# Optimization experiments

Measured on AMD Instinct MI355X. Metric: run time of the kernel, lower is better.

## Reference

```python
import jax, jax.numpy as jnp
import numpy as np
import math

B, T, D_IN, D_OUT = 4, 2048, 2048, 2048

def _inv_sigmoid(v):
    return math.log(v / (1 - v + 1e-08))

def setup_inputs() -> dict:
    key = jax.random.key(0)
    ks = jax.random.split(key, 6)
    x = jax.random.normal(ks[0], (B, T, D_IN), dtype=jnp.float32)
    W_p = jax.random.normal(ks[1], (D_OUT, D_IN), dtype=jnp.float32) * 0.02
    W_i = jax.random.normal(ks[2], (D_OUT, D_IN), dtype=jnp.float32) * 0.002
    W_d = jax.random.normal(ks[3], (D_OUT, D_IN), dtype=jnp.float32) * 0.002
    alpha_logit = jnp.full((D_IN,), _inv_sigmoid(0.9), dtype=jnp.float32)
    beta_logit = jnp.full((D_IN,), _inv_sigmoid(0.5), dtype=jnp.float32)
    W_gate_w = jax.random.normal(ks[4], (3, 3 * D_IN), dtype=jnp.float32) * 0.01
    W_gate_b = jnp.array([1.0, 0.0, 0.0], dtype=jnp.float32)
    bias = jnp.zeros((D_OUT,), dtype=jnp.float32)
    return {"x": x, "W_p": W_p, "W_i": W_i, "W_d": W_d,
            "alpha_logit": alpha_logit, "beta_logit": beta_logit,
            "W_gate_w": W_gate_w, "W_gate_b": W_gate_b, "bias": bias}

def _pid_features(x, alpha, beta):
    # x: (B,T,D). Single scan computing EMA integral and smoothed derivative.
    x_t = jnp.swapaxes(x, 0, 1)  # (T,B,D)
    x_prev = jnp.concatenate([jnp.zeros_like(x_t[:1]), x_t[:-1]], axis=0)
    diff_t = x_t - x_prev  # raw finite difference
    def step(carry, inp):
        s, d = carry
        xt, dt = inp
        s = alpha * s + (1.0 - alpha) * xt
        d = beta * d + (1.0 - beta) * dt
        return (s, d), (s, d)
    s0 = jnp.zeros(x.shape[::2], dtype=x.dtype)  # (B,D)
    _, (integ_t, deriv_t) = jax.lax.scan(step, (s0, s0), (x_t, diff_t))
    return jnp.swapaxes(integ_t, 0, 1), jnp.swapaxes(deriv_t, 0, 1)

def reference(x, W_p, W_i, W_d, alpha_logit, beta_logit, W_gate_w, W_gate_b, bias):
    alpha = jax.nn.sigmoid(alpha_logit)  # (D,)
    beta = jax.nn.sigmoid(beta_logit)
    integral, derivative = _pid_features(x, alpha, beta)  # (B,T,D) each
    gate_in = jnp.concatenate([x, integral, derivative], axis=-1)  # (B,T,3D)
    logits = jnp.einsum('btk,gk->btg', gate_in, W_gate_w) + W_gate_b
    gates = jax.nn.softmax(logits, axis=-1)  # (B,T,3)
    p_out = jnp.einsum('btd,od->bto', x, W_p)
    i_out = jnp.einsum('btd,od->bto', integral, W_i)
    d_out = jnp.einsum('btd,od->bto', derivative, W_d)
    y = gates[..., 0:1] * p_out + gates[..., 1:2] * i_out + gates[..., 2:3] * d_out + bias
    return y
```

## Files before the change

### kernel.cpp

```cpp
#include <hip/hip_runtime.h>
#include <stdint.h>

typedef unsigned short u16;

#define GAS __attribute__((address_space(1)))
#define LAS __attribute__((address_space(3)))

typedef __bf16 bf16x8 __attribute__((ext_vector_type(8)));
typedef float f32x4 __attribute__((ext_vector_type(4)));


__device__ inline u16 f2b(float f) {
    uint32_t x = __float_as_uint(f);
    uint32_t r = (x + 0x7fffu + ((x >> 16) & 1u)) >> 16;
    return (u16)r;
}

__device__ inline float b2f(u16 u) {
    union { uint32_t i; float f; } v;
    v.i = ((uint32_t)u) << 16;
    return v.f;
}

__device__ inline void load8b(float* v, const u16* p) {
    uint4 u = *(const uint4*)p;
    v[0] = b2f((u16)(u.x)); v[1] = b2f((u16)(u.x >> 16));
    v[2] = b2f((u16)(u.y)); v[3] = b2f((u16)(u.y >> 16));
    v[4] = b2f((u16)(u.z)); v[5] = b2f((u16)(u.z >> 16));
    v[6] = b2f((u16)(u.w)); v[7] = b2f((u16)(u.w >> 16));
}

__device__ inline void load8f(float* v, const float* p) {
    float4 a = *(const float4*)p;
    float4 b = *(const float4*)(p + 4);
    v[0] = a.x; v[1] = a.y; v[2] = a.z; v[3] = a.w;
    v[4] = b.x; v[5] = b.y; v[6] = b.z; v[7] = b.w;
}

__device__ inline void store8b(u16* p, const float* v, float scale) {
    uint4 u;
    u.x = (uint32_t)f2b(v[0] * scale) | ((uint32_t)f2b(v[1] * scale) << 16);
    u.y = (uint32_t)f2b(v[2] * scale) | ((uint32_t)f2b(v[3] * scale) << 16);
    u.z = (uint32_t)f2b(v[4] * scale) | ((uint32_t)f2b(v[5] * scale) << 16);
    u.w = (uint32_t)f2b(v[6] * scale) | ((uint32_t)f2b(v[7] * scale) << 16);
    *(uint4*)p = u;
}

__device__ inline float sigmoidf(float v) { return 1.f / (1.f + __expf(-v)); }

__device__ inline float pow64f(float a) {
    float p = a * a;
    p = p * p;
    p = p * p;
    p = p * p;
    p = p * p;
    return p * p;
}

__device__ inline float* carry_ptr(u16* Z, int plane, int b, int c, int d) {
    int f = ((plane * 4 + b) * 32 + c) * 2048 + d;
    int row = f >> 10;
    int off = f & 1023;
    return (float*)(Z + (size_t)row * 6144) + off;
}

__global__ __launch_bounds__(256) void pack_w(
    const float* __restrict__ Wp, const float* __restrict__ Wi,
    const float* __restrict__ Wd, u16* __restrict__ Wcat)
{
    int i = (blockIdx.x * 256 + threadIdx.x) * 8;
    int seg = i >> 22;
    int j = i & 4194303;
    const float* src = (seg == 0) ? Wp : (seg == 1) ? Wi : Wd;
    int o = j >> 11;
    int c = j & 2047;
    float v[8];
    load8f(v, src + j);
    store8b(Wcat + (size_t)o * 6144 + seg * 2048 + c, v, 1.0f);
}

__global__ __launch_bounds__(256) void scan_pass1(
    const float* __restrict__ x, const float* __restrict__ alog,
    const float* __restrict__ blog, u16* __restrict__ Z)
{
    const int d = blockIdx.x * 256 + threadIdx.x;
    const int c = blockIdx.y;
    const int b = blockIdx.z;
    const float alpha = sigmoidf(alog[d]);
    const float beta  = sigmoidf(blog[d]);
    const float oma = 1.f - alpha, omb = 1.f - beta;
    const float* xp = x + ((size_t)b * 2048 + c * 64) * 2048 + d;
    float xprev = (c == 0) ? 0.f : xp[-2048];
    float s = 0.f, dd = 0.f;
    #pragma unroll 8
    for (int t = 0; t < 64; ++t) {
        float xf = xp[(size_t)t * 2048];
        s = alpha * s + oma * xf;
        dd = beta * dd + omb * (xf - xprev);
        xprev = xf;
    }
    *carry_ptr(Z, 0, b, c, d) = s;
    *carry_ptr(Z, 1, b, c, d) = dd;
}

__global__ __launch_bounds__(256) void scan_pass2(
    const float* __restrict__ alog, const float* __restrict__ blog,
    u16* __restrict__ Z)
{
    const int g = blockIdx.x * 256 + threadIdx.x;
    const int b = g >> 11;
    const int d = g & 2047;
    const float aL = pow64f(sigmoidf(alog[d]));
    const float bL = pow64f(sigmoidf(blog[d]));
    float sIn = 0.f, dIn = 0.f;
    for (int c = 0; c < 32; ++c) {
        float* sp = carry_ptr(Z, 0, b, c, d);
        float* dp = carry_ptr(Z, 1, b, c, d);
        float sl = *sp, dl = *dp;
        *sp = sIn; *dp = dIn;
        sIn = sl + aL * sIn;
        dIn = dl + bL * dIn;
    }
}

__global__ __launch_bounds__(256) void scan_pass3(
    const float* __restrict__ x, const float* __restrict__ alog,
    const float* __restrict__ blog, u16* __restrict__ Z)
{
    const int d = blockIdx.x * 256 + threadIdx.x;
    const int c = blockIdx.y;
    const int b = blockIdx.z;
    const float alpha = sigmoidf(alog[d]);
    const float beta  = sigmoidf(blog[d]);
    const float oma = 1.f - alpha, omb = 1.f - beta;
    const float* xp = x + ((size_t)b * 2048 + c * 64) * 2048 + d;
    u16* zp = Z + ((size_t)b * 2048 + c * 64) * 6144 + 2048 + d;
    float s  = *carry_ptr(Z, 0, b, c, d);
    float dd = *carry_ptr(Z, 1, b, c, d);
    float xprev = (c == 0) ? 0.f : xp[-2048];
    #pragma unroll 8
    for (int t = 0; t < 64; ++t) {
        float xf = xp[(size_t)t * 2048];
        s = alpha * s + oma * xf;
        dd = beta * dd + omb * (xf - xprev);
        xprev = xf;
        size_t zo = (size_t)t * 6144;
        zp[zo] = f2b(s);
        zp[zo + 2048] = f2b(dd);
    }
}

__global__ __launch_bounds__(256) void gates_kernel(
    const float* __restrict__ x, const float* __restrict__ Wg,
    const float* __restrict__ Wgb, u16* __restrict__ Z)
{
    const int row = blockIdx.x;
    const int tid = threadIdx.x;
    const int k = tid * 8;
    const float* xr = x + (size_t)row * 2048;
    u16* zr = Z + (size_t)row * 6144;

    float xv[8], sv[8], dv[8];
    load8f(xv, xr + k);
    load8b(sv, zr + 2048 + k);
    load8b(dv, zr + 4096 + k);

    float p[3];
    #pragma unroll
    for (int gg = 0; gg < 3; ++gg) {
        float wx[8], ws[8], wd[8];
        load8f(wx, Wg + gg * 6144 + k);
        load8f(ws, Wg + gg * 6144 + 2048 + k);
        load8f(wd, Wg + gg * 6144 + 4096 + k);
        float acc = 0.f;
        #pragma unroll
        for (int j = 0; j < 8; ++j)
            acc += xv[j] * wx[j] + sv[j] * ws[j] + dv[j] * wd[j];
        p[gg] = acc;
    }

    #pragma unroll
    for (int off = 32; off > 0; off >>= 1) {
        p[0] += __shfl_down(p[0], off);
        p[1] += __shfl_down(p[1], off);
        p[2] += __shfl_down(p[2], off);
    }

    __shared__ float red[4][3];
    __shared__ float gsh[3];
    int wv = tid >> 6, lane = tid & 63;
    if (lane == 0) { red[wv][0] = p[0]; red[wv][1] = p[1]; red[wv][2] = p[2]; }
    __syncthreads();
    if (tid == 0) {
        float l0 = red[0][0] + red[1][0] + red[2][0] + red[3][0] + Wgb[0];
        float l1 = red[0][1] + red[1][1] + red[2][1] + red[3][1] + Wgb[1];
        float l2 = red[0][2] + red[1][2] + red[2][2] + red[3][2] + Wgb[2];
        float m = fmaxf(l0, fmaxf(l1, l2));
        float e0 = __expf(l0 - m), e1 = __expf(l1 - m), e2 = __expf(l2 - m);
        float inv = 1.f / (e0 + e1 + e2);
        gsh[0] = e0 * inv; gsh[1] = e1 * inv; gsh[2] = e2 * inv;
    }
    __syncthreads();
    float g0 = gsh[0], g1 = gsh[1], g2 = gsh[2];
    store8b(zr + k, xv, g0);
    store8b(zr + 2048 + k, sv, g1);
    store8b(zr + 4096 + k, dv, g2);
}

__global__ __launch_bounds__(256, 3) void gemm_kernel(
    const u16* __restrict__ Z, const u16* __restrict__ Wcat,
    const float* __restrict__ bias, float* __restrict__ out)
{
    __shared__ u16 a_sh[128 * 64];
    __shared__ u16 b_sh[128 * 64];

    const int tid = threadIdx.x;
    const int bm = blockIdx.y * 128;
    const int bn = blockIdx.x * 128;

    const int srow = tid >> 3;
    const int scq  = tid & 7;
    const int ssub = (scq ^ (srow & 7)) * 8;
    const u16* aglob = Z + (size_t)(bm + srow) * 6144 + ssub;
    const u16* bglob = Wcat + (size_t)(bn + srow) * 6144 + ssub;
    u16* alds[4];
    u16* blds[4];
    #pragma unroll
    for (int c = 0; c < 4; ++c) {
        alds[c] = a_sh + c * 2048 + tid * 8;
        blds[c] = b_sh + c * 2048 + tid * 8;
    }

    const int lane = tid & 63;
    const int wv = tid >> 6;
    const int wm = (wv & 1) * 64;
    const int wn = (wv >> 1) * 64;
    const int fr = lane & 15;
    const int fq = lane >> 4;

    f32x4 acc[4][4] = {};

    for (int kt = 0; kt < 96; ++kt) {
        const int k0 = kt * 64;
        #pragma unroll
        for (int c = 0; c < 4; ++c)
            __builtin_amdgcn_global_load_lds(
                (const GAS uint32_t*)(aglob + (size_t)c * 32 * 6144 + k0),
                (LAS uint32_t*)alds[c], 16, 0, 0);
        #pragma unroll
        for (int c = 0; c < 4; ++c)
            __builtin_amdgcn_global_load_lds(
                (const GAS uint32_t*)(bglob + (size_t)c * 32 * 6144 + k0),
                (LAS uint32_t*)blds[c], 16, 0, 0);
        __syncthreads();

        #pragma unroll
        for (int h = 0; h < 2; ++h) {
            bf16x8 avf[4], bvf[4];
            #pragma unroll
            for (int i = 0; i < 4; ++i) {
                int row = wm + i * 16 + fr;
                int ch = (fq + 4 * h) ^ (row & 7);
                avf[i] = *(const bf16x8*)(a_sh + row * 64 + ch * 8);
            }
            #pragma unroll
            for (int j = 0; j < 4; ++j) {
                int row = wn + j * 16 + fr;
                int ch = (fq + 4 * h) ^ (row & 7);
                bvf[j] = *(const bf16x8*)(b_sh + row * 64 + ch * 8);
            }
            #pragma unroll
            for (int i = 0; i < 4; ++i)
                #pragma unroll
                for (int j = 0; j < 4; ++j)
                    acc[i][j] = __builtin_amdgcn_mfma_f32_16x16x32_bf16(
                        avf[i], bvf[j], acc[i][j], 0, 0, 0);
        }
        __syncthreads();
    }

    #pragma unroll
    for (int j = 0; j < 4; ++j) {
        const int col = bn + wn + j * 16 + fr;
        const float bv = bias[col];
        #pragma unroll
        for (int i = 0; i < 4; ++i) {
            const int row0 = bm + wm + i * 16 + fq * 4;
            #pragma unroll
            for (int r = 0; r < 4; ++r)
                out[(size_t)(row0 + r) * 2048 + col] = acc[i][j][r] + bv;
        }
    }
}

extern "C" void kernel_launch(void* const* d_in, const int* in_sizes, int n_in,
                              void* d_out, int out_size, void* d_ws, size_t ws_size,
                              hipStream_t stream) {
    const float* x    = (const float*)d_in[0];
    const float* Wp   = (const float*)d_in[1];
    const float* Wi   = (const float*)d_in[2];
    const float* Wd   = (const float*)d_in[3];
    const float* al   = (const float*)d_in[4];
    const float* bl   = (const float*)d_in[5];
    const float* Wg   = (const float*)d_in[6];
    const float* Wgb  = (const float*)d_in[7];
    const float* bias = (const float*)d_in[8];
    float* out = (float*)d_out;

    u16* Z    = (u16*)d_ws;
    u16* Wcat = (u16*)((char*)d_ws + (size_t)8192 * 6144 * 2);

    pack_w<<<6144, 256, 0, stream>>>(Wp, Wi, Wd, Wcat);
    scan_pass1<<<dim3(8, 32, 4), 256, 0, stream>>>(x, al, bl, Z);
    scan_pass2<<<32, 256, 0, stream>>>(al, bl, Z);
    scan_pass3<<<dim3(8, 32, 4), 256, 0, stream>>>(x, al, bl, Z);
    gates_kernel<<<8192, 256, 0, stream>>>(x, Wg, Wgb, Z);
    gemm_kernel<<<dim3(16, 64), 256, 0, stream>>>(Z, Wcat, bias, out);
}
```

Measured before the change: 442.7 us.

## Fuse gate logits into scan pass and apply gates as GEMM epilogue scaling

Removes the separate gates kernel. The scan now writes x, integral and derivative as unscaled bf16 into Z and accumulates the gate logits through wave reductions and atomics. A small softmax kernel turns the logits into gates. The GEMM applies the per-row gates by rescaling the accumulators between K segments with ratios g0/g1 and g1/g2, then multiplying by g2 in the epilogue. This avoids one full read and rewrite of Z, at the cost of per-timestep wave shuffles and atomics in the scan, plus division-based rescaling that can lose precision or blow up when a gate is tiny.

```diff
diff --git a/kernel.cpp b/kernel.cpp
--- a/kernel.cpp
+++ b/kernel.cpp
@@ -14,20 +14,6 @@
     uint32_t x = __float_as_uint(f);
     uint32_t r = (x + 0x7fffu + ((x >> 16) & 1u)) >> 16;
     return (u16)r;
-}
-
-__device__ inline float b2f(u16 u) {
-    union { uint32_t i; float f; } v;
-    v.i = ((uint32_t)u) << 16;
-    return v.f;
-}
-
-__device__ inline void load8b(float* v, const u16* p) {
-    uint4 u = *(const uint4*)p;
-    v[0] = b2f((u16)(u.x)); v[1] = b2f((u16)(u.x >> 16));
-    v[2] = b2f((u16)(u.y)); v[3] = b2f((u16)(u.y >> 16));
-    v[4] = b2f((u16)(u.z)); v[5] = b2f((u16)(u.z >> 16));
-    v[6] = b2f((u16)(u.w)); v[7] = b2f((u16)(u.w >> 16));
 }
 
 __device__ inline void load8f(float* v, const float* p) {
@@ -37,12 +23,12 @@
     v[4] = b.x; v[5] = b.y; v[6] = b.z; v[7] = b.w;
 }
 
-__device__ inline void store8b(u16* p, const float* v, float scale) {
+__device__ inline void store8b(u16* p, const float* v) {
     uint4 u;
-    u.x = (uint32_t)f2b(v[0] * scale) | ((uint32_t)f2b(v[1] * scale) << 16);
-    u.y = (uint32_t)f2b(v[2] * scale) | ((uint32_t)f2b(v[3] * scale) << 16);
-    u.z = (uint32_t)f2b(v[4] * scale) | ((uint32_t)f2b(v[5] * scale) << 16);
-    u.w = (uint32_t)f2b(v[6] * scale) | ((uint32_t)f2b(v[7] * scale) << 16);
+    u.x = (uint32_t)f2b(v[0]) | ((uint32_t)f2b(v[1]) << 16);
+    u.y = (uint32_t)f2b(v[2]) | ((uint32_t)f2b(v[3]) << 16);
+    u.z = (uint32_t)f2b(v[4]) | ((uint32_t)f2b(v[5]) << 16);
+    u.w = (uint32_t)f2b(v[6]) | ((uint32_t)f2b(v[7]) << 16);
     *(uint4*)p = u;
 }
 
@@ -55,13 +41,6 @@
     p = p * p;
     p = p * p;
     return p * p;
-}
-
-__device__ inline float* carry_ptr(u16* Z, int plane, int b, int c, int d) {
-    int f = ((plane * 4 + b) * 32 + c) * 2048 + d;
-    int row = f >> 10;
-    int off = f & 1023;
-    return (float*)(Z + (size_t)row * 6144) + off;
 }
 
 __global__ __launch_bounds__(256) void pack_w(
@@ -76,12 +55,12 @@
     int c = j & 2047;
     float v[8];
     load8f(v, src + j);
-    store8b(Wcat + (size_t)o * 6144 + seg * 2048 + c, v, 1.0f);
+    store8b(Wcat + (size_t)o * 6144 + seg * 2048 + c, v);
 }
 
 __global__ __launch_bounds__(256) void scan_pass1(
     const float* __restrict__ x, const float* __restrict__ alog,
-    const float* __restrict__ blog, u16* __restrict__ Z)
+    const float* __restrict__ blog, float* __restrict__ carries)
 {
     const int d = blockIdx.x * 256 + threadIdx.x;
     const int c = blockIdx.y;
@@ -99,13 +78,13 @@
         dd = beta * dd + omb * (xf - xprev);
         xprev = xf;
     }
-    *carry_ptr(Z, 0, b, c, d) = s;
-    *carry_ptr(Z, 1, b, c, d) = dd;
+    carries[((0 * 4 + b) * 32 + c) * 2048 + d] = s;
+    carries[((1 * 4 + b) * 32 + c) * 2048 + d] = dd;
 }
 
 __global__ __launch_bounds__(256) void scan_pass2(
     const float* __restrict__ alog, const float* __restrict__ blog,
-    u16* __restrict__ Z)
+    float* __restrict__ carries)
 {
     const int g = blockIdx.x * 256 + threadIdx.x;
     const int b = g >> 11;
@@ -114,8 +93,8 @@
     const float bL = pow64f(sigmoidf(blog[d]));
     float sIn = 0.f, dIn = 0.f;
     for (int c = 0; c < 32; ++c) {
-        float* sp = carry_ptr(Z, 0, b, c, d);
-        float* dp = carry_ptr(Z, 1, b, c, d);
+        float* sp = carries + ((0 * 4 + b) * 32 + c) * 2048 + d;
+        float* dp = carries + ((1 * 4 + b) * 32 + c) * 2048 + d;
         float sl = *sp, dl = *dp;
         *sp = sIn; *dp = dIn;
         sIn = sl + aL * sIn;
@@ -125,7 +104,9 @@
 
 __global__ __launch_bounds__(256) void scan_pass3(
     const float* __restrict__ x, const float* __restrict__ alog,
-    const float* __restrict__ blog, u16* __restrict__ Z)
+    const float* __restrict__ blog, const float* __restrict__ Wg,
+    const float* __restrict__ carries, u16* __restrict__ Z,
+    float* __restrict__ logits)
 {
     const int d = blockIdx.x * 256 + threadIdx.x;
     const int c = blockIdx.y;
@@ -133,83 +114,63 @@
     const float alpha = sigmoidf(alog[d]);
     const float beta  = sigmoidf(blog[d]);
     const float oma = 1.f - alpha, omb = 1.f - beta;
+    const float w0x = Wg[d],         w0s = Wg[2048 + d],         w0d = Wg[4096 + d];
+    const float w1x = Wg[6144 + d],  w1s = Wg[6144 + 2048 + d],  w1d = Wg[6144 + 4096 + d];
+    const float w2x = Wg[12288 + d], w2s = Wg[12288 + 2048 + d], w2d = Wg[12288 + 4096 + d];
     const float* xp = x + ((size_t)b * 2048 + c * 64) * 2048 + d;
-    u16* zp = Z + ((size_t)b * 2048 + c * 64) * 6144 + 2048 + d;
-    float s  = *carry_ptr(Z, 0, b, c, d);
-    float dd = *carry_ptr(Z, 1, b, c, d);
+    u16* zp = Z + ((size_t)b * 2048 + c * 64) * 6144 + d;
+    float s  = carries[((0 * 4 + b) * 32 + c) * 2048 + d];
+    float dd = carries[((1 * 4 + b) * 32 + c) * 2048 + d];
     float xprev = (c == 0) ? 0.f : xp[-2048];
-    #pragma unroll 8
+    const int rowbase = b * 2048 + c * 64;
+    const int lane = threadIdx.x & 63;
+    #pragma unroll 4
     for (int t = 0; t < 64; ++t) {
         float xf = xp[(size_t)t * 2048];
         s = alpha * s + oma * xf;
         dd = beta * dd + omb * (xf - xprev);
         xprev = xf;
         size_t zo = (size_t)t * 6144;
-        zp[zo] = f2b(s);
-        zp[zo + 2048] = f2b(dd);
-    }
-}
-
-__global__ __launch_bounds__(256) void gates_kernel(
-    const float* __restrict__ x, const float* __restrict__ Wg,
-    const float* __restrict__ Wgb, u16* __restrict__ Z)
-{
-    const int row = blockIdx.x;
-    const int tid = threadIdx.x;
-    const int k = tid * 8;
-    const float* xr = x + (size_t)row * 2048;
-    u16* zr = Z + (size_t)row * 6144;
-
-    float xv[8], sv[8], dv[8];
-    load8f(xv, xr + k);
-    load8b(sv, zr + 2048 + k);
-    load8b(dv, zr + 4096 + k);
-
-    float p[3];
-    #pragma unroll
-    for (int gg = 0; gg < 3; ++gg) {
-        float wx[8], ws[8], wd[8];
-        load8f(wx, Wg + gg * 6144 + k);
-        load8f(ws, Wg + gg * 6144 + 2048 + k);
-        load8f(wd, Wg + gg * 6144 + 4096 + k);
-        float acc = 0.f;
+        zp[zo]        = f2b(xf);
+        zp[zo + 2048] = f2b(s);
+        zp[zo + 4096] = f2b(dd);
+        float c0 = w0x * xf + w0s * s + w0d * dd;
+        float c1 = w1x * xf + w1s * s + w1d * dd;
+        float c2 = w2x * xf + w2s * s + w2d * dd;
         #pragma unroll
-        for (int j = 0; j < 8; ++j)
-            acc += xv[j] * wx[j] + sv[j] * ws[j] + dv[j] * wd[j];
-        p[gg] = acc;
-    }
-
-    #pragma unroll
-    for (int off = 32; off > 0; off >>= 1) {
-        p[0] += __shfl_down(p[0], off);
-        p[1] += __shfl_down(p[1], off);
-        p[2] += __shfl_down(p[2], off);
-    }
-
-    __shared__ float red[4][3];
-    __shared__ float gsh[3];
-    int wv = tid >> 6, lane = tid & 63;
-    if (lane == 0) { red[wv][0] = p[0]; red[wv][1] = p[1]; red[wv][2] = p[2]; }
-    __syncthreads();
-    if (tid == 0) {
-        float l0 = red[0][0] + red[1][0] + red[2][0] + red[3][0] + Wgb[0];
-        float l1 = red[0][1] + red[1][1] + red[2][1] + red[3][1] + Wgb[1];
-        float l2 = red[0][2] + red[1][2] + red[2][2] + red[3][2] + Wgb[2];
-        float m = fmaxf(l0, fmaxf(l1, l2));
-        float e0 = __expf(l0 - m), e1 = __expf(l1 - m), e2 = __expf(l2 - m);
-        float inv = 1.f / (e0 + e1 + e2);
-        gsh[0] = e0 * inv; gsh[1] = e1 * inv; gsh[2] = e2 * inv;
-    }
-    __syncthreads();
-    float g0 = gsh[0], g1 = gsh[1], g2 = gsh[2];
-    store8b(zr + k, xv, g0);
-    store8b(zr + 2048 + k, sv, g1);
-    store8b(zr + 4096 + k, dv, g2);
+        for (int off = 32; off > 0; off >>= 1) {
+            c0 += __shfl_xor(c0, off);
+            c1 += __shfl_xor(c1, off);
+            c2 += __shfl_xor(c2, off);
+        }
+        if (lane == 0) {
+            int row = rowbase + t;
+            atomicAdd(&logits[row * 3 + 0], c0);
+            atomicAdd(&logits[row * 3 + 1], c1);
+            atomicAdd(&logits[row * 3 + 2], c2);
+        }
+    }
+}
+
+__global__ __launch_bounds__(256) void softmax_k(
+    float* __restrict__ logits, const float* __restrict__ Wgb)
+{
+    int r = blockIdx.x * 256 + threadIdx.x;
+    float l0 = logits[r * 3 + 0] + Wgb[0];
+    float l1 = logits[r * 3 + 1] + Wgb[1];
+    float l2 = logits[r * 3 + 2] + Wgb[2];
+    float m = fmaxf(l0, fmaxf(l1, l2));
+    float e0 = __expf(l0 - m), e1 = __expf(l1 - m), e2 = __expf(l2 - m);
+    float inv = 1.f / (e0 + e1 + e2);
+    logits[r * 3 + 0] = e0 * inv;
+    logits[r * 3 + 1] = e1 * inv;
+    logits[r * 3 + 2] = e2 * inv;
 }
 
 __global__ __launch_bounds__(256, 3) void gemm_kernel(
     const u16* __restrict__ Z, const u16* __restrict__ Wcat,
-    const float* __restrict__ bias, float* __restrict__ out)
+    const float* __restrict__ gates, const float* __restrict__ bias,
+    float* __restrict__ out)
 {
     __shared__ u16 a_sh[128 * 64];
     __shared__ u16 b_sh[128 * 64];
@@ -238,45 +199,74 @@
     const int fr = lane & 15;
     const int fq = lane >> 4;
 
+    float r01[16], r12[16], g2v[16];
+    #pragma unroll
+    for (int i = 0; i < 4; ++i) {
+        #pragma unroll
+        for (int r = 0; r < 4; ++r) {
+            int row = bm + wm + i * 16 + fq * 4 + r;
+            float g0 = gates[row * 3 + 0];
+            float g1 = gates[row * 3 + 1];
+            float g2 = gates[row * 3 + 2];
+            int idx = i * 4 + r;
+            r01[idx] = g0 / g1;
+            r12[idx] = g1 / g2;
+            g2v[idx] = g2;
+        }
+    }
+
     f32x4 acc[4][4] = {};
 
-    for (int kt = 0; kt < 96; ++kt) {
-        const int k0 = kt * 64;
-        #pragma unroll
-        for (int c = 0; c < 4; ++c)
-            __builtin_amdgcn_global_load_lds(
-                (const GAS uint32_t*)(aglob + (size_t)c * 32 * 6144 + k0),
-                (LAS uint32_t*)alds[c], 16, 0, 0);
-        #pragma unroll
-        for (int c = 0; c < 4; ++c)
-            __builtin_amdgcn_global_load_lds(
-                (const GAS uint32_t*)(bglob + (size_t)c * 32 * 6144 + k0),
-                (LAS uint32_t*)blds[c], 16, 0, 0);
-        __syncthreads();
-
-        #pragma unroll
-        for (int h = 0; h < 2; ++h) {
-            bf16x8 avf[4], bvf[4];
-            #pragma unroll
-            for (int i = 0; i < 4; ++i) {
-                int row = wm + i * 16 + fr;
-                int ch = (fq + 4 * h) ^ (row & 7);
-                avf[i] = *(const bf16x8*)(a_sh + row * 64 + ch * 8);
+    for (int seg = 0; seg < 3; ++seg) {
+        for (int kt = 0; kt < 32; ++kt) {
+            const int k0 = seg * 2048 + kt * 64;
+            #pragma unroll
+            for (int c = 0; c < 4; ++c)
+                __builtin_amdgcn_global_load_lds(
+                    (const GAS uint32_t*)(aglob + (size_t)c * 32 * 6144 + k0),
+                    (LAS uint32_t*)alds[c], 16, 0, 0);
+            #pragma unroll
+            for (int c = 0; c < 4; ++c)
+                __builtin_amdgcn_global_load_lds(
+                    (const GAS uint32_t*)(bglob + (size_t)c * 32 * 6144 + k0),
+                    (LAS uint32_t*)blds[c], 16, 0, 0);
+            __syncthreads();
+
+            #pragma unroll
+            for (int h = 0; h < 2; ++h) {
+                bf16x8 avf[4], bvf[4];
+                #pragma unroll
+                for (int i = 0; i < 4; ++i) {
+                    int row = wm + i * 16 + fr;
+                    int ch = (fq + 4 * h) ^ (row & 7);
+                    avf[i] = *(const bf16x8*)(a_sh + row * 64 + ch * 8);
+                }
+                #pragma unroll
+                for (int j = 0; j < 4; ++j) {
+                    int row = wn + j * 16 + fr;
+                    int ch = (fq + 4 * h) ^ (row & 7);
+                    bvf[j] = *(const bf16x8*)(b_sh + row * 64 + ch * 8);
+                }
+                #pragma unroll
+                for (int i = 0; i < 4; ++i)
+                    #pragma unroll
+                    for (int j = 0; j < 4; ++j)
+                        acc[i][j] = __builtin_amdgcn_mfma_f32_16x16x32_bf16(
+                            avf[i], bvf[j], acc[i][j], 0, 0, 0);
             }
-            #pragma unroll
-            for (int j = 0; j < 4; ++j) {
-                int row = wn + j * 16 + fr;
-                int ch = (fq + 4 * h) ^ (row & 7);
-                bvf[j] = *(const bf16x8*)(b_sh + row * 64 + ch * 8);
-            }
+            __syncthreads();
+        }
+        if (seg < 2) {
             #pragma unroll
             for (int i = 0; i < 4; ++i)
                 #pragma unroll
-                for (int j = 0; j < 4; ++j)
-                    acc[i][j] = __builtin_amdgcn_mfma_f32_16x16x32_bf16(
-                        avf[i], bvf[j], acc[i][j], 0, 0, 0);
-        }
-        __syncthreads();
+                for (int r = 0; r < 4; ++r) {
+                    float sc = (seg == 0) ? r01[i * 4 + r] : r12[i * 4 + r];
+                    #pragma unroll
+                    for (int j = 0; j < 4; ++j)
+                        acc[i][j][r] *= sc;
+                }
+        }
     }
 
     #pragma unroll
@@ -288,7 +278,8 @@
             const int row0 = bm + wm + i * 16 + fq * 4;
             #pragma unroll
             for (int r = 0; r < 4; ++r)
-                out[(size_t)(row0 + r) * 2048 + col] = acc[i][j][r] + bv;
+                out[(size_t)(row0 + r) * 2048 + col] =
+                    acc[i][j][r] * g2v[i * 4 + r] + bv;
         }
     }
 }
@@ -307,13 +298,16 @@
     const float* bias = (const float*)d_in[8];
     float* out = (float*)d_out;
 
-    u16* Z    = (u16*)d_ws;
-    u16* Wcat = (u16*)((char*)d_ws + (size_t)8192 * 6144 * 2);
-
+    u16* Z       = (u16*)d_ws;
+    u16* Wcat    = (u16*)((char*)d_ws + (size_t)8192 * 6144 * 2);
+    float* carries = (float*)Wcat;
+    float* logits  = (float*)((char*)d_ws + (size_t)10240 * 6144 * 2);
+
+    hipMemsetAsync(logits, 0, (size_t)8192 * 3 * sizeof(float), stream);
+    scan_pass1<<<dim3(8, 32, 4), 256, 0, stream>>>(x, al, bl, carries);
+    scan_pass2<<<32, 256, 0, stream>>>(al, bl, carries);
+    scan_pass3<<<dim3(8, 32, 4), 256, 0, stream>>>(x, al, bl, Wg, carries, Z, logits);
+    softmax_k<<<32, 256, 0, stream>>>(logits, Wgb);
     pack_w<<<6144, 256, 0, stream>>>(Wp, Wi, Wd, Wcat);
-    scan_pass1<<<dim3(8, 32, 4), 256, 0, stream>>>(x, al, bl, Z);
-    scan_pass2<<<32, 256, 0, stream>>>(al, bl, Z);
-    scan_pass3<<<dim3(8, 32, 4), 256, 0, stream>>>(x, al, bl, Z);
-    gates_kernel<<<8192, 256, 0, stream>>>(x, Wg, Wgb, Z);
-    gemm_kernel<<<dim3(16, 64), 256, 0, stream>>>(Z, Wcat, bias, out);
-}
+    gemm_kernel<<<dim3(16, 64), 256, 0, stream>>>(Z, Wcat, logits, bias, out);
+}
```

Result: slower. 525.2 us (+18.6%).
